# Performance work log

Hardware: AMD Instinct MI355X
Metric: run time of the kernel (lower is better)

## Reference

```python
import jax, jax.numpy as jnp
import numpy as np

# --- static config (matches init_kwargs) ---
B, S, DIM = 1, 2048, 1024
H, G, DK, DV = 16, 4, 64, 64
HPG = H // G
L, D, LSEL, NSEL, W = 32, 16, 64, 16, 512
NCMP = (S - L) // D + 1            # number of compressed blocks over full prefill
J = S // LSEL                      # number of selection blocks
GH = 32                            # gate hidden
NEG = -1e30


def rope(x, pos):
    # x: [B, S, N, Dh]; llama-style half rotation
    Dh = x.shape[-1]
    inv = 1.0 / (10000.0 ** (np.arange(0, Dh, 2) / Dh))
    ang = pos[:, None] * inv[None, :]                      # [S, Dh/2]
    cos = jnp.asarray(np.cos(ang), jnp.float32)[None, :, None, :]
    sin = jnp.asarray(np.sin(ang), jnp.float32)[None, :, None, :]
    x1, x2 = jnp.split(x, 2, axis=-1)
    return jnp.concatenate([x1 * cos - x2 * sin, x2 * cos + x1 * sin], axis=-1)


def masked_softmax(s, m):
    p = jax.nn.softmax(jnp.where(m, s, NEG), axis=-1)
    # rows with no visible keys produce 0 output (empty attention)
    return jnp.where(jnp.any(m, axis=-1, keepdims=True), p, 0.0)


def setup_inputs() -> dict:
    key = jax.random.key(0)
    ks = jax.random.split(key, 12)
    def w(k, shape, fan):
        return jax.random.normal(k, shape, jnp.float32) / np.sqrt(fan)
    return {
        'x': jax.random.normal(ks[0], (B, S, DIM), jnp.float32),
        'W_Q': w(ks[1], (DIM, H * DK), DIM),
        'W_K_sel': w(ks[2], (DIM, G * DK), DIM),
        'W_V_sel': w(ks[3], (DIM, G * DV), DIM),
        'W_K_win': w(ks[4], (DIM, G * DK), DIM),
        'W_V_win': w(ks[5], (DIM, G * DV), DIM),
        'W_K_cmp': w(ks[6], (DIM, G * DK), DIM),
        'W_V_cmp': w(ks[7], (DIM, G * DV), DIM),
        'W_out': w(ks[8], (H * DV, DIM), H * DV),
        'gate_w1': w(ks[9], (DK, GH), DK),
        'gate_b1': jnp.zeros((GH,), jnp.float32),
        'gate_w2': 0.1 * jax.random.normal(ks[10], (GH, 3), jnp.float32),
        'gate_b2': jnp.zeros((3,), jnp.float32),
    }


def reference(x, W_Q, W_K_sel, W_V_sel, W_K_win, W_V_win, W_K_cmp, W_V_cmp,
              W_out, gate_w1, gate_b1, gate_w2, gate_b2):
    pos = np.arange(S)
    s_ = np.arange(S)
    scale = 1.0 / np.sqrt(DK)

    Q = rope((x @ W_Q).reshape(B, S, H, DK), pos).reshape(B, S, G, HPG, DK)

    def proj_kv(Wk, Wv):
        K = rope((x @ Wk).reshape(B, S, G, DK), pos).transpose(0, 2, 1, 3)  # [B,G,S,Dk]
        V = (x @ Wv).reshape(B, S, G, DV).transpose(0, 2, 1, 3)            # [B,G,S,Dv]
        return K, V

    K_sel, V_sel = proj_kv(W_K_sel, W_V_sel)
    K_win, V_win = proj_kv(W_K_win, W_V_win)
    K_cr, V_cr = proj_kv(W_K_cmp, W_V_cmp)

    # --- compressed branch: avg-pool (len L, stride D) of roped K / raw V ---
    bidx = np.arange(NCMP)[:, None] * D + np.arange(L)[None, :]   # [NCMP, L]
    K_cmp = K_cr[:, :, bidx].mean(axis=3)                         # [B,G,NCMP,Dk]
    V_cmp = V_cr[:, :, bidx].mean(axis=3)
    vis_c = (np.arange(NCMP)[None, :] * D + L) <= (s_[:, None] + 1)  # block fully in past
    sc_c = jnp.einsum('bsghd,bgcd->bsghc', Q, K_cmp) * scale
    p_cmp = masked_softmax(sc_c, jnp.asarray(vis_c)[None, :, None, None, :])
    O_cmp = jnp.einsum('bsghc,bgce->bsghe', p_cmp, V_cmp)

    # --- map compressed probs -> selection-block scores (overlap fractions) ---
    i0 = np.arange(NCMP)[:, None] * D
    j0 = np.arange(J)[None, :] * LSEL
    ov = np.maximum(0, np.minimum(i0 + L, j0 + LSEL) - np.maximum(i0, j0)) / L
    p_grp = jnp.einsum('bsghc,cj->bsgj', p_cmp, jnp.asarray(ov, np.float32))  # sum over heads in group

    vis_j = (np.arange(J)[None, :] * LSEL) <= s_[:, None]
    forced = (np.arange(J)[None, :] == 0) | (np.arange(J)[None, :] == (s_ // LSEL)[:, None])
    score = jnp.where(jnp.asarray(vis_j)[None, :, None, :], p_grp, NEG)
    score = jnp.where(jnp.asarray(forced)[None, :, None, :], 1e9, score)  # force block 0 + current block
    topj = jax.lax.top_k(score, NSEL)[1]                                   # [B,S,G,NSEL]
    blk = jax.nn.one_hot(topj, J, dtype=jnp.float32).sum(axis=-2) > 0      # [B,S,G,J]

    tok2blk = np.repeat(np.arange(J), LSEL)[:S]
    causal = s_[:, None] >= s_[None, :]                                    # u <= t
    sel_mask = blk[:, :, :, tok2blk] & jnp.asarray(causal)[None, :, None, :]  # [B,S,G,S]
    sc_s = jnp.einsum('bsghd,bgud->bsghu', Q, K_sel) * scale
    O_sel = jnp.einsum('bsghu,bgue->bsghe',
                       masked_softmax(sc_s, sel_mask[:, :, :, None, :]), V_sel)

    # --- sliding window branch ---
    win_mask = causal & (s_[None, :] > s_[:, None] - W)
    sc_w = jnp.einsum('bsghd,bgud->bsghu', Q, K_win) * scale
    O_win = jnp.einsum('bsghu,bgue->bsghe',
                       masked_softmax(sc_w, jnp.asarray(win_mask)[None, :, None, None, :]), V_win)

    # --- gating MLP on head-pooled query per group ---
    gl = jax.nn.silu(Q.mean(axis=3) @ gate_w1 + gate_b1) @ gate_w2 + gate_b2  # [B,S,G,3]
    pg = jax.nn.softmax(gl, axis=-1)
    t2 = jax.lax.top_k(gl, 2)[0]
    peaked = (t2[..., 0] - t2[..., 1]) > 50.0
    gates = jnp.where(peaked[..., None],
                      jax.nn.one_hot(jnp.argmax(gl, axis=-1), 3, dtype=gl.dtype), pg)

    O = (gates[..., 0, None, None] * O_cmp
         + gates[..., 1, None, None] * O_sel
         + gates[..., 2, None, None] * O_win)          # [B,S,G,h,Dv]
    return O.reshape(B, S, H * DV) @ W_out
```

## Files before the change

### kernel.cpp

```cpp
#include <hip/hip_runtime.h>
#include <math.h>

#define S 2048
#define DIM 1024
#define H 16
#define G 4
#define HPG 4
#define DK 64
#define DV 64
#define NCMP 127
#define JBLK 32
#define NSEL 16
#define WWIN 512
#define GH 32
#define SCL2 0.18033688011112042f

typedef __attribute__((ext_vector_type(8))) __bf16 bf16x8;
typedef __attribute__((ext_vector_type(4))) float f32x4;

__device__ __forceinline__ unsigned short f2bf(float f) {
  unsigned u = __float_as_uint(f);
  unsigned r = (u + 0x7FFFu + ((u >> 16) & 1u)) >> 16;
  return (unsigned short)r;
}

__device__ __forceinline__ unsigned short f2bf_hw(float f) {
  __bf16 b = (__bf16)f;
  return *(unsigned short*)&b;
}

__device__ __forceinline__ float bf2f(unsigned short u) {
  return __uint_as_float((unsigned)u << 16);
}

__device__ __forceinline__ f32x4 mfma16(bf16x8 a, bf16x8 b, f32x4 c) {
  return __builtin_amdgcn_mfma_f32_16x16x32_bf16(a, b, c, 0, 0, 0);
}

__global__ void rope_table(float* __restrict__ cosT, float* __restrict__ sinT) {
  int idx = blockIdx.x * blockDim.x + threadIdx.x;
  if (idx >= S * 32) return;
  int s = idx >> 5, i = idx & 31;
  double inv = pow(10000.0, -2.0 * (double)i / 64.0);
  double ang = (double)s * inv;
  cosT[idx] = (float)cos(ang);
  sinT[idx] = (float)sin(ang);
}

__device__ __forceinline__ void gemm_body_k(const float* __restrict__ A,
                                            const float* __restrict__ B,
                                            float* __restrict__ C,
                                            int N, int K, int bm, int bn,
                                            int kS, int kE,
                                            float* As, float* Bs) {
  int tid = threadIdx.x;
  int tr = tid >> 4, tc = tid & 15;
  float acc[4][4] = {{0.f}};
  int arow = tid >> 2;
  int kba = (tid & 3) << 3;
  int brow = tid >> 4;
  int bcol = (tid & 15) << 2;
  const float* Ab = A + (size_t)(bm * 64) * K;
  const float* Bb = B + bn * 64;

  float4 a0 = *(const float4*)(Ab + (size_t)arow * K + kS + kba);
  float4 a1 = *(const float4*)(Ab + (size_t)arow * K + kS + kba + 4);
  float4 b0 = *(const float4*)(Bb + (size_t)(kS + brow) * N + bcol);
  float4 b1 = *(const float4*)(Bb + (size_t)(kS + brow + 16) * N + bcol);

  for (int k0 = kS; k0 < kE; k0 += 32) {
    __syncthreads();
    {
      float av[8] = {a0.x, a0.y, a0.z, a0.w, a1.x, a1.y, a1.z, a1.w};
#pragma unroll
      for (int i = 0; i < 8; ++i) {
        int k = kba + i;
        As[k * 64 + (arow ^ (((k >> 3) & 3) << 3))] = av[i];
      }
      *(float4*)&Bs[brow * 64 + bcol] = b0;
      *(float4*)&Bs[(brow + 16) * 64 + bcol] = b1;
    }
    __syncthreads();
    if (k0 + 32 < kE) {
      a0 = *(const float4*)(Ab + (size_t)arow * K + k0 + 32 + kba);
      a1 = *(const float4*)(Ab + (size_t)arow * K + k0 + 32 + kba + 4);
      b0 = *(const float4*)(Bb + (size_t)(k0 + 32 + brow) * N + bcol);
      b1 = *(const float4*)(Bb + (size_t)(k0 + 32 + brow + 16) * N + bcol);
    }
#pragma unroll
    for (int kk = 0; kk < 32; ++kk) {
      float4 a = *(const float4*)&As[kk * 64 + ((tr << 2) ^ (((kk >> 3) & 3) << 3))];
      float4 b = *(const float4*)&Bs[kk * 64 + (tc << 2)];
      acc[0][0] += a.x * b.x; acc[0][1] += a.x * b.y; acc[0][2] += a.x * b.z; acc[0][3] += a.x * b.w;
      acc[1][0] += a.y * b.x; acc[1][1] += a.y * b.y; acc[1][2] += a.y * b.z; acc[1][3] += a.y * b.w;
      acc[2][0] += a.z * b.x; acc[2][1] += a.z * b.y; acc[2][2] += a.z * b.z; acc[2][3] += a.z * b.w;
      acc[3][0] += a.w * b.x; acc[3][1] += a.w * b.y; acc[3][2] += a.w * b.z; acc[3][3] += a.w * b.w;
    }
  }
  for (int i = 0; i < 4; ++i)
    for (int jj = 0; jj < 4; ++jj)
      C[(size_t)(bm * 64 + (tr << 2) + i) * N + bn * 64 + (tc << 2) + jj] = acc[i][jj];
}

__global__ __launch_bounds__(256) void gemm_qk(const float* __restrict__ x,
                                               const float* __restrict__ W_Q,
                                               const float* __restrict__ W_Kc,
                                               float* __restrict__ Pq,
                                               float* __restrict__ Pk) {
  __shared__ float As[32 * 64];
  __shared__ float Bs[32 * 64];
  int ct = blockIdx.x, bm = blockIdx.y, z = blockIdx.z;
  int kS = z * 512, kE = kS + 512;
  if (ct < 16)
    gemm_body_k(x, W_Q, Pq + (size_t)z * S * 1024, 1024, DIM, bm, ct, kS, kE, As, Bs);
  else
    gemm_body_k(x, W_Kc, Pk + (size_t)z * S * 256, 256, DIM, bm, ct - 16, kS, kE, As, Bs);
}

__global__ __launch_bounds__(256) void reduce_rope(
    const float* __restrict__ Pq, const float* __restrict__ Pk,
    const float* __restrict__ cosT, const float* __restrict__ sinT,
    float* __restrict__ Qb, unsigned short* __restrict__ Qbf,
    float* __restrict__ Kcr) {
  int idx = blockIdx.x * 256 + threadIdx.x;
  const int NQ = S * H * 32;
  if (idx < NQ) {
    int i = idx & 31;
    int rest = idx >> 5;
    int h = rest & 15;
    int s = rest >> 4;
    size_t base = (size_t)s * 1024 + h * 64 + i;
    float a1 = Pq[base] + Pq[(size_t)S * 1024 + base];
    float a2 = Pq[base + 32] + Pq[(size_t)S * 1024 + base + 32];
    float c = cosT[s * 32 + i], sn = sinT[s * 32 + i];
    float q1 = a1 * c - a2 * sn, q2 = a2 * c + a1 * sn;
    Qb[base] = q1;
    Qb[base + 32] = q2;
    Qbf[base] = f2bf(q1);
    Qbf[base + 32] = f2bf(q2);
  } else {
    int j = idx - NQ;
    if (j >= S * G * 32) return;
    int i = j & 31;
    int rest = j >> 5;
    int g = rest & 3;
    int s = rest >> 2;
    size_t base = (size_t)s * 256 + g * 64 + i;
    float a1 = Pk[base] + Pk[(size_t)S * 256 + base];
    float a2 = Pk[base + 32] + Pk[(size_t)S * 256 + base + 32];
    float c = cosT[s * 32 + i], sn = sinT[s * 32 + i];
    Kcr[base] = a1 * c - a2 * sn;
    Kcr[base + 32] = a2 * c + a1 * sn;
  }
}

__global__ __launch_bounds__(256) void fconv(const float* __restrict__ a,
                                             unsigned short* __restrict__ b) {
  int idx = (blockIdx.x * 256 + threadIdx.x) * 8;
  float4 x = *(const float4*)&a[idx];
  float4 y = *(const float4*)&a[idx + 4];
  union { unsigned short us[8]; float4 f4; } t;
  t.us[0] = f2bf(x.x); t.us[1] = f2bf(x.y); t.us[2] = f2bf(x.z); t.us[3] = f2bf(x.w);
  t.us[4] = f2bf(y.x); t.us[5] = f2bf(y.y); t.us[6] = f2bf(y.z); t.us[7] = f2bf(y.w);
  *(float4*)&b[idx] = t.f4;
}

__global__ __launch_bounds__(256) void wtrans(const float* __restrict__ W0,
                                              const float* __restrict__ W1,
                                              const float* __restrict__ W2,
                                              const float* __restrict__ W3,
                                              const float* __restrict__ W4,
                                              unsigned short* __restrict__ Wt) {
  __shared__ float t[64][65];
  int k0 = blockIdx.x * 64;
  int n0 = blockIdx.y * 64;
  int m = blockIdx.z;
  const float* W = (m == 0) ? W0 : (m == 1) ? W1 : (m == 2) ? W2 : (m == 3) ? W3 : W4;
  int tid = threadIdx.x;
  int rr = tid >> 4, c4 = (tid & 15) * 4;
#pragma unroll
  for (int e = 0; e < 4; ++e) {
    int row = rr + e * 16;
    float4 v = *(const float4*)(W + (size_t)(k0 + row) * 256 + n0 + c4);
    t[c4 + 0][row] = v.x;
    t[c4 + 1][row] = v.y;
    t[c4 + 2][row] = v.z;
    t[c4 + 3][row] = v.w;
  }
  __syncthreads();
#pragma unroll
  for (int e = 0; e < 2; ++e) {
    int flat = tid + e * 256;
    int col = flat >> 3, kc = (flat & 7) * 8;
    union { unsigned short us[8]; float4 f4; } u;
#pragma unroll
    for (int i = 0; i < 8; ++i) u.us[i] = f2bf(t[col][kc + i]);
    *(float4*)(Wt + ((size_t)m * 256 + n0 + col) * 1024 + k0 + kc) = u.f4;
  }
}

__global__ __launch_bounds__(256) void wtrans_o(const float* __restrict__ W,
                                                unsigned short* __restrict__ Wt) {
  __shared__ float t[64][65];
  int k0 = blockIdx.x * 64;
  int n0 = blockIdx.y * 64;
  int tid = threadIdx.x;
  int rr = tid >> 4, c4 = (tid & 15) * 4;
#pragma unroll
  for (int e = 0; e < 4; ++e) {
    int row = rr + e * 16;
    float4 v = *(const float4*)(W + (size_t)(k0 + row) * 1024 + n0 + c4);
    t[c4 + 0][row] = v.x;
    t[c4 + 1][row] = v.y;
    t[c4 + 2][row] = v.z;
    t[c4 + 3][row] = v.w;
  }
  __syncthreads();
#pragma unroll
  for (int e = 0; e < 2; ++e) {
    int flat = tid + e * 256;
    int col = flat >> 3, kc = (flat & 7) * 8;
    union { unsigned short us[8]; float4 f4; } u;
#pragma unroll
    for (int i = 0; i < 8; ++i) u.us[i] = f2bf(t[col][kc + i]);
    *(float4*)(Wt + (size_t)(n0 + col) * 1024 + k0 + kc) = u.f4;
  }
}

__global__ __launch_bounds__(256) void proj_bf16(
    const unsigned short* __restrict__ xb, const unsigned short* __restrict__ Wt,
    const float* __restrict__ cosT, const float* __restrict__ sinT,
    unsigned short* __restrict__ Kb_s, unsigned short* __restrict__ Vt_s,
    unsigned short* __restrict__ Kb_w, unsigned short* __restrict__ Vt_w,
    unsigned short* __restrict__ Vt_c) {
  __shared__ unsigned short xs[64 * 64];
  __shared__ unsigned short ws[64 * 64];
  int s0 = blockIdx.x * 64;
  int g = blockIdx.y;
  int mat = blockIdx.z;
  int tid = threadIdx.x, w = tid >> 6, lane = tid & 63;
  int l15 = lane & 15, lg = lane >> 4;
  int rswz = (l15 & 7) << 3;
  bool isV = (mat == 1) || (mat == 3) || (mat == 4);
  const unsigned short* wt = Wt + ((size_t)mat * 256 + g * 64) * 1024;

  f32x4 acc[4];
#pragma unroll
  for (int nt = 0; nt < 4; ++nt) acc[nt] = (f32x4){0.f, 0.f, 0.f, 0.f};

  for (int k0 = 0; k0 < DIM; k0 += 64) {
#pragma unroll
    for (int e = 0; e < 2; ++e) {
      int flat = tid + e * 256;
      int row = flat >> 3, cc = flat & 7;
      int dsti = row * 64 + ((cc ^ (row & 7)) << 3);
      *(float4*)&xs[dsti] = *(const float4*)(xb + (size_t)(s0 + row) * DIM + k0 + cc * 8);
      *(float4*)&ws[dsti] = *(const float4*)(wt + (size_t)row * DIM + k0 + cc * 8);
    }
    __syncthreads();
    const unsigned short* aP = isV ? ws : xs;
    const unsigned short* bP = isV ? xs : ws;
    int arow = w * 16 + l15;
    bf16x8 af[2];
#pragma unroll
    for (int kc = 0; kc < 2; ++kc)
      af[kc] = *(const bf16x8*)&aP[(arow * 64 + kc * 32 + lg * 8) ^ rswz];
#pragma unroll
    for (int nt = 0; nt < 4; ++nt) {
      int brow = nt * 16 + l15;
      bf16x8 b0 = *(const bf16x8*)&bP[(brow * 64 + lg * 8) ^ rswz];
      bf16x8 b1 = *(const bf16x8*)&bP[(brow * 64 + 32 + lg * 8) ^ rswz];
      acc[nt] = mfma16(af[0], b0, acc[nt]);
      acc[nt] = mfma16(af[1], b1, acc[nt]);
    }
    __syncthreads();
  }

  if (!isV) {
    unsigned short* Kb = (mat == 0) ? Kb_s : Kb_w;
#pragma unroll
    for (int rr = 0; rr < 4; ++rr) {
      int tok = s0 + w * 16 + lg * 4 + rr;
#pragma unroll
      for (int p = 0; p < 2; ++p) {
        int i = p * 16 + l15;
        float c = cosT[tok * 32 + i], sn = sinT[tok * 32 + i];
        float x1 = acc[p][rr], x2 = acc[p + 2][rr];
        Kb[((size_t)g * S + tok) * 64 + i] = f2bf(x1 * c - x2 * sn);
        Kb[((size_t)g * S + tok) * 64 + i + 32] = f2bf(x2 * c + x1 * sn);
      }
    }
  } else {
    unsigned short* Vt = (mat == 1) ? Vt_s : (mat == 3) ? Vt_w : Vt_c;
#pragma unroll
    for (int rr = 0; rr < 4; ++rr) {
      int col = w * 16 + lg * 4 + rr;
#pragma unroll
      for (int nt = 0; nt < 4; ++nt) {
        int tok = s0 + nt * 16 + l15;
        Vt[((size_t)g * 64 + col) * S + tok] = f2bf(acc[nt][rr]);
      }
    }
  }
}

__global__ __launch_bounds__(256) void gemm_out(const unsigned short* __restrict__ Ob,
                                                const unsigned short* __restrict__ Wt,
                                                float* __restrict__ out) {
  __shared__ unsigned short xs[64 * 64];
  __shared__ unsigned short ws[64 * 64];
  int s0 = blockIdx.x * 64;
  int n0 = blockIdx.y * 64;
  int tid = threadIdx.x, w = tid >> 6, lane = tid & 63;
  int l15 = lane & 15, lg = lane >> 4;
  int rswz = (l15 & 7) << 3;

  f32x4 acc[4];
#pragma unroll
  for (int nt = 0; nt < 4; ++nt) acc[nt] = (f32x4){0.f, 0.f, 0.f, 0.f};

  for (int k0 = 0; k0 < DIM; k0 += 64) {
#pragma unroll
    for (int e = 0; e < 2; ++e) {
      int flat = tid + e * 256;
      int row = flat >> 3, cc = flat & 7;
      int dsti = row * 64 + ((cc ^ (row & 7)) << 3);
      *(float4*)&xs[dsti] = *(const float4*)(Ob + (size_t)(s0 + row) * DIM + k0 + cc * 8);
      *(float4*)&ws[dsti] = *(const float4*)(Wt + (size_t)(n0 + row) * DIM + k0 + cc * 8);
    }
    __syncthreads();
    int arow = w * 16 + l15;
    bf16x8 af0 = *(const bf16x8*)&xs[(arow * 64 + lg * 8) ^ rswz];
    bf16x8 af1 = *(const bf16x8*)&xs[(arow * 64 + 32 + lg * 8) ^ rswz];
#pragma unroll
    for (int nt = 0; nt < 4; ++nt) {
      int brow = nt * 16 + l15;
      bf16x8 b0 = *(const bf16x8*)&ws[(brow * 64 + lg * 8) ^ rswz];
      bf16x8 b1 = *(const bf16x8*)&ws[(brow * 64 + 32 + lg * 8) ^ rswz];
      acc[nt] = mfma16(af0, b0, acc[nt]);
      acc[nt] = mfma16(af1, b1, acc[nt]);
    }
    __syncthreads();
  }

#pragma unroll
  for (int nt = 0; nt < 4; ++nt)
#pragma unroll
    for (int rr = 0; rr < 4; ++rr)
      out[(size_t)(s0 + w * 16 + lg * 4 + rr) * 1024 + n0 + nt * 16 + l15] =
          acc[nt][rr];
}

__global__ void pool_cmp(const float* __restrict__ Kcr,
                         const unsigned short* __restrict__ Vtc,
                         float* __restrict__ Kc, float* __restrict__ Vc) {
  int c = blockIdx.x, g = blockIdx.y, d = threadIdx.x;
  float sk = 0.f, sv = 0.f;
  const unsigned short* vrow = Vtc + ((size_t)g * 64 + d) * S + c * 16;
  for (int l = 0; l < 32; ++l) {
    sk += Kcr[(size_t)((c * 16 + l) * G + g) * 64 + d];
    sv += bf2f(vrow[l]);
  }
  Kc[(size_t)(g * NCMP + c) * 64 + d] = sk * (1.f / 32.f);
  Vc[(size_t)(g * NCMP + c) * 64 + d] = sv * (1.f / 32.f);
}

__global__ __launch_bounds__(256) void cmp_attn(const float* __restrict__ Q,
                                                const float* __restrict__ Kc,
                                                const float* __restrict__ Vc,
                                                float* __restrict__ Ocmp,
                                                unsigned int* __restrict__ selm) {
  int s = blockIdx.x, g = blockIdx.y;
  __shared__ float q4[4][64];
  __shared__ float sc[4][128];
  __shared__ float pg[JBLK];
  int tid = threadIdx.x;
  int nvis = (s >= 31) ? (((s - 31) >> 4) + 1) : 0;
  {
    int h = tid >> 6, d = tid & 63;
    q4[h][d] = Q[(size_t)(s * H + g * HPG + h) * 64 + d];
  }
  __syncthreads();

  if (tid < 128) {
    int c = tid;
    if (c < nvis) {
      float a0 = 0.f, a1 = 0.f, a2 = 0.f, a3 = 0.f;
      const float* kr = &Kc[(size_t)(g * NCMP + c) * 64];
#pragma unroll 4
      for (int kk = 0; kk < 16; ++kk) {
        float4 kv = *(const float4*)&kr[kk * 4];
        float4 q0 = *(const float4*)&q4[0][kk * 4];
        float4 q1 = *(const float4*)&q4[1][kk * 4];
        float4 q2 = *(const float4*)&q4[2][kk * 4];
        float4 q3 = *(const float4*)&q4[3][kk * 4];
        a0 += q0.x * kv.x + q0.y * kv.y + q0.z * kv.z + q0.w * kv.w;
        a1 += q1.x * kv.x + q1.y * kv.y + q1.z * kv.z + q1.w * kv.w;
        a2 += q2.x * kv.x + q2.y * kv.y + q2.z * kv.z + q2.w * kv.w;
        a3 += q3.x * kv.x + q3.y * kv.y + q3.z * kv.z + q3.w * kv.w;
      }
      sc[0][c] = a0 * 0.125f;
      sc[1][c] = a1 * 0.125f;
      sc[2][c] = a2 * 0.125f;
      sc[3][c] = a3 * 0.125f;
    } else {
      sc[0][c] = -INFINITY;
      sc[1][c] = -INFINITY;
      sc[2][c] = -INFINITY;
      sc[3][c] = -INFINITY;
    }
  }
  __syncthreads();

  int w = tid >> 6, lane = tid & 63;
  {
    float v0 = sc[w][lane];
    float v1 = (lane + 64 < NCMP) ? sc[w][lane + 64] : -INFINITY;
    float m = fmaxf(v0, v1);
    for (int off = 32; off; off >>= 1) m = fmaxf(m, __shfl_xor(m, off));
    float e0 = (m > -INFINITY && v0 > -INFINITY) ? expf(v0 - m) : 0.f;
    float e1 = (m > -INFINITY && v1 > -INFINITY) ? expf(v1 - m) : 0.f;
    float sum = e0 + e1;
    for (int off = 32; off; off >>= 1) sum += __shfl_xor(sum, off);
    float inv = (sum > 0.f) ? 1.f / sum : 0.f;
    sc[w][lane] = e0 * inv;
    if (lane + 64 < NCMP) sc[w][lane + 64] = e1 * inv;
    if (lane == 63) sc[w][127] = 0.f;
  }
  __syncthreads();

  {
    int h = tid >> 6, d = tid & 63;
    float o = 0.f;
#pragma unroll 4
    for (int c = 0; c < nvis; ++c) o += sc[h][c] * Vc[(size_t)(g * NCMP + c) * 64 + d];
    Ocmp[(size_t)(s * H + g * HPG + h) * 64 + d] = o;
  }

  if (tid < JBLK) {
    int j = tid;
    float a = 0.f;
#pragma unroll
    for (int h = 0; h < 4; ++h) {
      const float* row = sc[h];
      float v = row[4 * j] + row[4 * j + 1] + row[4 * j + 2] + 0.5f * row[4 * j + 3];
      if (j > 0) v += 0.5f * row[4 * j - 1];
      a += v;
    }
    pg[j] = a;
  }
  __syncthreads();

  if (tid < 64) {
    int j = tid & 31;
    int cur = s >> 6;
    float v = (j * 64 <= s) ? pg[j] : -1e30f;
    if (j == 0 || j == cur) v = 1e9f;
    unsigned int mask = 0;
#pragma unroll 1
    for (int n = 0; n < NSEL; ++n) {
      float bv = v;
      int bj = j;
#pragma unroll
      for (int off = 1; off < 32; off <<= 1) {
        float ov = __shfl_xor(bv, off);
        int oj = __shfl_xor(bj, off);
        if (ov > bv || (ov == bv && oj < bj)) { bv = ov; bj = oj; }
      }
      mask |= 1u << bj;
      if (j == bj) v = -INFINITY;
    }
    if (tid == 0) selm[(size_t)s * G + g] = mask;
  }
}

__global__ __launch_bounds__(256) void attn_fused(
    const unsigned short* __restrict__ Qbf,
    const unsigned short* __restrict__ Kbs, const unsigned short* __restrict__ Vts,
    const unsigned short* __restrict__ Kbw, const unsigned short* __restrict__ Vtw,
    const unsigned int* __restrict__ selm,
    float* __restrict__ Osel, float* __restrict__ Owin) {
  __shared__ unsigned short Kl[64 * 64];
  __shared__ unsigned short Vt[64 * 64];
  __shared__ unsigned short Pl[4][16 * 64];
  __shared__ unsigned int sel_l[16];
  __shared__ int blist[JBLK];
  __shared__ int nB_s;

  int t0 = blockIdx.x * 16;
  int g = blockIdx.y;
  int mode = blockIdx.z;
  int tid = threadIdx.x;
  int w = tid >> 6, lane = tid & 63;
  int l15 = lane & 15, lg = lane >> 4;
  int rswz = (l15 & 7) << 3;
  int jdiag = t0 >> 6;

  const unsigned short* Kb = mode ? Kbw : Kbs;
  const unsigned short* Vtb = mode ? Vtw : Vts;
  float* O = mode ? Owin : Osel;

  if (mode == 0 && tid < 16) sel_l[tid] = selm[(t0 + tid) * G + g];
  __syncthreads();
  if (tid == 0) {
    int n = 0;
    if (mode == 0) {
      unsigned int un = 0;
      for (int i = 0; i < 16; ++i) un |= sel_l[i];
      for (int j = 0; j <= jdiag; ++j)
        if ((un >> j) & 1u) blist[n++] = j;
    } else {
      int lo = t0 - (WWIN - 1);
      int j0 = (lo > 0) ? (lo >> 6) : 0;
      for (int j = j0; j <= jdiag; ++j) blist[n++] = j;
    }
    nB_s = n;
  }
  __syncthreads();
  int nB = nB_s;

  int tok = t0 + l15;
  bf16x8 qf[2];
  {
    const unsigned short* qb = Qbf + ((size_t)tok * H + g * HPG + w) * 64;
    qf[0] = *(const bf16x8*)(qb + lg * 8);
    qf[1] = *(const bf16x8*)(qb + 32 + lg * 8);
  }

  float mrun = -INFINITY, lrun = 0.f;
  f32x4 oacc[4];
#pragma unroll
  for (int dt = 0; dt < 4; ++dt) oacc[dt] = (f32x4){0.f, 0.f, 0.f, 0.f};

  for (int b = 0; b < nB; ++b) {
    int j = blist[b];
    int ku = j * 64;

    {
      const unsigned short* src = Kb + ((size_t)g * S + ku) * 64;
#pragma unroll
      for (int c2 = 0; c2 < 2; ++c2) {
        int chunk = tid + c2 * 256;
        int key = chunk >> 3, cc = chunk & 7;
        *(float4*)&Kl[key * 64 + ((cc ^ (key & 7)) << 3)] =
            *(const float4*)(src + chunk * 8);
      }
#pragma unroll
      for (int c2 = 0; c2 < 2; ++c2) {
        int chunk = tid + c2 * 256;
        int dim = chunk >> 3, cc = chunk & 7;
        *(float4*)&Vt[dim * 64 + ((cc ^ (dim & 7)) << 3)] =
            *(const float4*)(Vtb + ((size_t)g * 64 + dim) * S + ku + cc * 8);
      }
    }
    __syncthreads();

    f32x4 sf[4];
#pragma unroll
    for (int kt = 0; kt < 4; ++kt) sf[kt] = (f32x4){0.f, 0.f, 0.f, 0.f};
#pragma unroll
    for (int kt = 0; kt < 4; ++kt) {
      int krow = kt * 16 + l15;
      bf16x8 kf0 = *(const bf16x8*)&Kl[(krow * 64 + lg * 8) ^ rswz];
      bf16x8 kf1 = *(const bf16x8*)&Kl[(krow * 64 + 32 + lg * 8) ^ rswz];
      sf[kt] = mfma16(kf0, qf[0], sf[kt]);
      sf[kt] = mfma16(kf1, qf[1], sf[kt]);
    }

    bool bsel = true;
    if (mode == 0) bsel = ((sel_l[l15] >> j) & 1u) != 0;
    float sv2[4][4];
    if (j == jdiag) {
#pragma unroll
      for (int kt = 0; kt < 4; ++kt)
#pragma unroll
        for (int rr = 0; rr < 4; ++rr) {
          int u = ku + kt * 16 + lg * 4 + rr;
          sv2[kt][rr] = (u <= tok) ? sf[kt][rr] * SCL2 : -INFINITY;
        }
    } else if (mode == 1 && (ku + WWIN <= t0 + 15)) {
#pragma unroll
      for (int kt = 0; kt < 4; ++kt)
#pragma unroll
        for (int rr = 0; rr < 4; ++rr) {
          int u = ku + kt * 16 + lg * 4 + rr;
          sv2[kt][rr] = (u + WWIN > tok) ? sf[kt][rr] * SCL2 : -INFINITY;
        }
    } else {
#pragma unroll
      for (int kt = 0; kt < 4; ++kt)
#pragma unroll
        for (int rr = 0; rr < 4; ++rr) sv2[kt][rr] = sf[kt][rr] * SCL2;
    }

    float pmax = -INFINITY;
#pragma unroll
    for (int kt = 0; kt < 4; ++kt)
#pragma unroll
      for (int rr = 0; rr < 4; ++rr) pmax = fmaxf(pmax, sv2[kt][rr]);
    pmax = fmaxf(pmax, __shfl_xor(pmax, 16));
    pmax = fmaxf(pmax, __shfl_xor(pmax, 32));
    if (mode == 0 && !bsel) pmax = -INFINITY;

    if (__any(pmax > mrun)) {
      float mnew = fmaxf(mrun, pmax);
      float mc = (mnew == -INFINITY) ? 0.f : mnew;
      float fac = exp2f(mrun - mc);
      mrun = mnew;
      lrun *= fac;
#pragma unroll
      for (int dt = 0; dt < 4; ++dt)
#pragma unroll
        for (int rr = 0; rr < 4; ++rr) oacc[dt][rr] *= fac;
    }
    float mcb = (mode == 0 && !bsel) ? INFINITY
                                     : ((mrun == -INFINITY) ? 0.f : mrun);

    float psum = 0.f;
    unsigned short pb[16];
#pragma unroll
    for (int kt = 0; kt < 4; ++kt)
#pragma unroll
      for (int rr = 0; rr < 4; ++rr) {
        float e = exp2f(sv2[kt][rr] - mcb);
        psum += e;
        pb[kt * 4 + rr] = f2bf_hw(e);
      }
    psum += __shfl_xor(psum, 16);
    psum += __shfl_xor(psum, 32);
    lrun += psum;

    {
      unsigned short* pw = &Pl[w][0];
#pragma unroll
      for (int kt = 0; kt < 4; ++kt) {
        int idx = (l15 * 64 + kt * 16 + lg * 4) ^ rswz;
        unsigned int lo = (unsigned)pb[kt * 4] | ((unsigned)pb[kt * 4 + 1] << 16);
        unsigned int hi = (unsigned)pb[kt * 4 + 2] | ((unsigned)pb[kt * 4 + 3] << 16);
        *(uint2*)&pw[idx] = make_uint2(lo, hi);
      }
    }

#pragma unroll
    for (int kc = 0; kc < 2; ++kc) {
      bf16x8 pf = *(const bf16x8*)&Pl[w][(l15 * 64 + kc * 32 + lg * 8) ^ rswz];
#pragma unroll
      for (int dt = 0; dt < 4; ++dt) {
        bf16x8 vf = *(const bf16x8*)&Vt[((dt * 16 + l15) * 64 + kc * 32 + lg * 8) ^ rswz];
        oacc[dt] = mfma16(vf, pf, oacc[dt]);
      }
    }
    __syncthreads();
  }

  {
    float inv = (lrun > 0.f) ? 1.f / lrun : 0.f;
    float* ob = O + ((size_t)tok * H + g * HPG + w) * 64;
#pragma unroll
    for (int dt = 0; dt < 4; ++dt) {
      float4 v;
      v.x = oacc[dt][0] * inv;
      v.y = oacc[dt][1] * inv;
      v.z = oacc[dt][2] * inv;
      v.w = oacc[dt][3] * inv;
      *(float4*)(ob + dt * 16 + lg * 4) = v;
    }
  }
}

__global__ void gate_kernel(const float* __restrict__ Q, const float* __restrict__ w1,
                            const float* __restrict__ b1, const float* __restrict__ w2,
                            const float* __restrict__ b2, float* __restrict__ gates) {
  int idx = blockIdx.x * blockDim.x + threadIdx.x;
  if (idx >= S * G) return;
  int s = idx >> 2, g = idx & 3;
  float qm[64];
#pragma unroll
  for (int d = 0; d < 64; ++d) {
    float a = 0.f;
    for (int hp = 0; hp < HPG; ++hp) a += Q[(size_t)(s * H + g * HPG + hp) * 64 + d];
    qm[d] = a * 0.25f;
  }
  float gl[3] = {b2[0], b2[1], b2[2]};
  for (int j = 0; j < GH; ++j) {
    float z = b1[j];
    for (int d = 0; d < 64; ++d) z += qm[d] * w1[d * GH + j];
    float sl = z / (1.f + expf(-z));
    gl[0] += sl * w2[j * 3 + 0];
    gl[1] += sl * w2[j * 3 + 1];
    gl[2] += sl * w2[j * 3 + 2];
  }
  float m = fmaxf(gl[0], fmaxf(gl[1], gl[2]));
  float e0 = expf(gl[0] - m), e1 = expf(gl[1] - m), e2 = expf(gl[2] - m);
  float inv = 1.f / (e0 + e1 + e2);
  float p0 = e0 * inv, p1 = e1 * inv, p2 = e2 * inv;
  int am = (gl[0] >= gl[1] && gl[0] >= gl[2]) ? 0 : ((gl[1] >= gl[2]) ? 1 : 2);
  float t1 = (am == 0) ? fmaxf(gl[1], gl[2]) : ((am == 1) ? fmaxf(gl[0], gl[2]) : fmaxf(gl[0], gl[1]));
  if (m - t1 > 50.f) {
    p0 = (am == 0) ? 1.f : 0.f;
    p1 = (am == 1) ? 1.f : 0.f;
    p2 = (am == 2) ? 1.f : 0.f;
  }
  gates[idx * 3 + 0] = p0;
  gates[idx * 3 + 1] = p1;
  gates[idx * 3 + 2] = p2;
}

__global__ void combine(const float* __restrict__ Oc, const float* __restrict__ Os,
                        const float* __restrict__ Ow, const float* __restrict__ gates,
                        unsigned short* __restrict__ Ob) {
  int idx = blockIdx.x * blockDim.x + threadIdx.x;
  if (idx >= S * H * DV) return;
  int h = (idx >> 6) & 15;
  int s = idx >> 10;
  int g = h >> 2;
  const float* gp = &gates[(size_t)(s * G + g) * 3];
  Ob[idx] = f2bf(gp[0] * Oc[idx] + gp[1] * Os[idx] + gp[2] * Ow[idx]);
}

extern "C" void kernel_launch(void* const* d_in, const int* in_sizes, int n_in,
                              void* d_out, int out_size, void* d_ws, size_t ws_size,
                              hipStream_t stream) {
  const float* x = (const float*)d_in[0];
  const float* W_Q = (const float*)d_in[1];
  const float* W_K_sel = (const float*)d_in[2];
  const float* W_V_sel = (const float*)d_in[3];
  const float* W_K_win = (const float*)d_in[4];
  const float* W_V_win = (const float*)d_in[5];
  const float* W_K_cmp = (const float*)d_in[6];
  const float* W_V_cmp = (const float*)d_in[7];
  const float* W_out = (const float*)d_in[8];
  const float* gw1 = (const float*)d_in[9];
  const float* gb1 = (const float*)d_in[10];
  const float* gw2 = (const float*)d_in[11];
  const float* gb2 = (const float*)d_in[12];

  float* w = (float*)d_ws;
  float* cosT = w;  w += S * 32;
  float* sinT = w;  w += S * 32;
  float* Qb   = w;  w += S * H * DK;
  float* Kcr  = w;  w += S * G * DK;
  float* Kc   = w;  w += G * NCMP * DK;
  float* Vc   = w;  w += G * NCMP * DV;
  float* Ocmp = w;  w += S * H * DV;
  float* Osel = w;  w += S * H * DV;
  float* Owin = w;  w += S * H * DV;
  float* gates= w;  w += S * G * 3;
  unsigned int* selm = (unsigned int*)w;  w += S * G;
  unsigned short* Kbf_s = (unsigned short*)w;  w += (size_t)G * S * 64 / 2;
  unsigned short* Kbf_w = (unsigned short*)w;  w += (size_t)G * S * 64 / 2;
  unsigned short* Vt_s  = (unsigned short*)w;  w += (size_t)G * S * 64 / 2;
  unsigned short* Vt_w  = (unsigned short*)w;  w += (size_t)G * S * 64 / 2;
  unsigned short* Vt_c  = (unsigned short*)w;  w += (size_t)G * S * 64 / 2;
  unsigned short* Qbf   = (unsigned short*)w;  w += (size_t)S * H * 64 / 2;
  unsigned short* xb    = (unsigned short*)w;  w += (size_t)S * DIM / 2;
  unsigned short* Wt    = (unsigned short*)w;  w += (size_t)5 * 256 * DIM / 2;
  unsigned short* Ob    = (unsigned short*)w;  w += (size_t)S * H * DV / 2;
  unsigned short* WtO   = (unsigned short*)w;  w += (size_t)DIM * DIM / 2;

  float* Pq = Ocmp;
  float* Pk = Owin;

  rope_table<<<(S * 32 + 255) / 256, 256, 0, stream>>>(cosT, sinT);
  fconv<<<(S * DIM) / 2048, 256, 0, stream>>>(x, xb);
  wtrans<<<dim3(DIM / 64, 4, 5), 256, 0, stream>>>(W_K_sel, W_V_sel, W_K_win,
                                                   W_V_win, W_V_cmp, Wt);
  wtrans_o<<<dim3(DIM / 64, DIM / 64), 256, 0, stream>>>(W_out, WtO);

  gemm_qk<<<dim3(20, S / 64, 2), 256, 0, stream>>>(x, W_Q, W_K_cmp, Pq, Pk);
  reduce_rope<<<(S * (H + G) * 32) / 256, 256, 0, stream>>>(Pq, Pk, cosT, sinT,
                                                            Qb, Qbf, Kcr);

  proj_bf16<<<dim3(S / 64, G, 5), 256, 0, stream>>>(xb, Wt, cosT, sinT, Kbf_s, Vt_s,
                                                    Kbf_w, Vt_w, Vt_c);

  pool_cmp<<<dim3(NCMP, G), 64, 0, stream>>>(Kcr, Vt_c, Kc, Vc);

  cmp_attn<<<dim3(S, G), 256, 0, stream>>>(Qb, Kc, Vc, Ocmp, selm);
  attn_fused<<<dim3(S / 16, G, 2), 256, 0, stream>>>(Qbf, Kbf_s, Vt_s, Kbf_w, Vt_w,
                                                     selm, Osel, Owin);

  gate_kernel<<<(S * G + 255) / 256, 256, 0, stream>>>(Qb, gw1, gb1, gw2, gb2, gates);
  combine<<<(S * H * DV + 255) / 256, 256, 0, stream>>>(Ocmp, Osel, Owin, gates, Ob);

  gemm_out<<<dim3(S / 64, DIM / 64), 256, 0, stream>>>(Ob, WtO, (float*)d_out);
}
```

Baseline: 307.1 us.

## Fuse independent kernels into heterogeneous launches to overlap QK/proj and cmp/window attention

```diff
diff --git a/kernel.cpp b/kernel.cpp
--- a/kernel.cpp
+++ b/kernel.cpp
@@ -52,7 +52,7 @@
                                             float* __restrict__ C,
                                             int N, int K, int bm, int bn,
                                             int kS, int kE,
-                                            float* As, float* Bs) {
+                                            float* As , float* Bs ) {
   int tid = threadIdx.x;
   int tr = tid >> 4, tc = tid & 15;
   float acc[4][4] = {{0.f}};
@@ -102,19 +102,113 @@
       C[(size_t)(bm * 64 + (tr << 2) + i) * N + bn * 64 + (tc << 2) + jj] = acc[i][jj];
 }
 
-__global__ __launch_bounds__(256) void gemm_qk(const float* __restrict__ x,
-                                               const float* __restrict__ W_Q,
-                                               const float* __restrict__ W_Kc,
-                                               float* __restrict__ Pq,
-                                               float* __restrict__ Pk) {
-  __shared__ float As[32 * 64];
-  __shared__ float Bs[32 * 64];
-  int ct = blockIdx.x, bm = blockIdx.y, z = blockIdx.z;
-  int kS = z * 512, kE = kS + 512;
-  if (ct < 16)
-    gemm_body_k(x, W_Q, Pq + (size_t)z * S * 1024, 1024, DIM, bm, ct, kS, kE, As, Bs);
-  else
-    gemm_body_k(x, W_Kc, Pk + (size_t)z * S * 256, 256, DIM, bm, ct - 16, kS, kE, As, Bs);
+__device__ __forceinline__ void proj_body(
+    const unsigned short* __restrict__ xb, const unsigned short* __restrict__ Wt,
+    const float* __restrict__ cosT, const float* __restrict__ sinT,
+    unsigned short* __restrict__ Kb_s, unsigned short* __restrict__ Vt_s,
+    unsigned short* __restrict__ Kb_w, unsigned short* __restrict__ Vt_w,
+    unsigned short* __restrict__ Vt_c,
+    int s0, int g, int mat, unsigned short* xs, unsigned short* ws) {
+  int tid = threadIdx.x, w = tid >> 6, lane = tid & 63;
+  int l15 = lane & 15, lg = lane >> 4;
+  int rswz = (l15 & 7) << 3;
+  bool isV = (mat == 1) || (mat == 3) || (mat == 4);
+  const unsigned short* wt = Wt + ((size_t)mat * 256 + g * 64) * 1024;
+
+  f32x4 acc[4];
+#pragma unroll
+  for (int nt = 0; nt < 4; ++nt) acc[nt] = (f32x4){0.f, 0.f, 0.f, 0.f};
+
+  for (int k0 = 0; k0 < DIM; k0 += 64) {
+#pragma unroll
+    for (int e = 0; e < 2; ++e) {
+      int flat = tid + e * 256;
+      int row = flat >> 3, cc = flat & 7;
+      int dsti = row * 64 + ((cc ^ (row & 7)) << 3);
+      *(float4*)&xs[dsti] = *(const float4*)(xb + (size_t)(s0 + row) * DIM + k0 + cc * 8);
+      *(float4*)&ws[dsti] = *(const float4*)(wt + (size_t)row * DIM + k0 + cc * 8);
+    }
+    __syncthreads();
+    const unsigned short* aP = isV ? ws : xs;
+    const unsigned short* bP = isV ? xs : ws;
+    int arow = w * 16 + l15;
+    bf16x8 af[2];
+#pragma unroll
+    for (int kc = 0; kc < 2; ++kc)
+      af[kc] = *(const bf16x8*)&aP[(arow * 64 + kc * 32 + lg * 8) ^ rswz];
+#pragma unroll
+    for (int nt = 0; nt < 4; ++nt) {
+      int brow = nt * 16 + l15;
+      bf16x8 b0 = *(const bf16x8*)&bP[(brow * 64 + lg * 8) ^ rswz];
+      bf16x8 b1 = *(const bf16x8*)&bP[(brow * 64 + 32 + lg * 8) ^ rswz];
+      acc[nt] = mfma16(af[0], b0, acc[nt]);
+      acc[nt] = mfma16(af[1], b1, acc[nt]);
+    }
+    __syncthreads();
+  }
+
+  if (!isV) {
+    unsigned short* Kb = (mat == 0) ? Kb_s : Kb_w;
+#pragma unroll
+    for (int rr = 0; rr < 4; ++rr) {
+      int tok = s0 + w * 16 + lg * 4 + rr;
+#pragma unroll
+      for (int p = 0; p < 2; ++p) {
+        int i = p * 16 + l15;
+        float c = cosT[tok * 32 + i], sn = sinT[tok * 32 + i];
+        float x1 = acc[p][rr], x2 = acc[p + 2][rr];
+        Kb[((size_t)g * S + tok) * 64 + i] = f2bf(x1 * c - x2 * sn);
+        Kb[((size_t)g * S + tok) * 64 + i + 32] = f2bf(x2 * c + x1 * sn);
+      }
+    }
+  } else {
+    unsigned short* Vt = (mat == 1) ? Vt_s : (mat == 3) ? Vt_w : Vt_c;
+#pragma unroll
+    for (int rr = 0; rr < 4; ++rr) {
+      int col = w * 16 + lg * 4 + rr;
+#pragma unroll
+      for (int nt = 0; nt < 4; ++nt) {
+        int tok = s0 + nt * 16 + l15;
+        Vt[((size_t)g * 64 + col) * S + tok] = f2bf(acc[nt][rr]);
+      }
+    }
+  }
+}
+
+__global__ __launch_bounds__(256) void qk_proj(
+    const float* __restrict__ x, const float* __restrict__ W_Q,
+    const float* __restrict__ W_Kc, float* __restrict__ Pq, float* __restrict__ Pk,
+    const unsigned short* __restrict__ xb, const unsigned short* __restrict__ Wt,
+    const float* __restrict__ cosT, const float* __restrict__ sinT,
+    unsigned short* __restrict__ Kb_s, unsigned short* __restrict__ Vt_s,
+    unsigned short* __restrict__ Kb_w, unsigned short* __restrict__ Vt_w,
+    unsigned short* __restrict__ Vt_c) {
+  __shared__ __align__(16) float lds_f[4096];
+  int bid = blockIdx.x;
+  int r = bid % 3;
+  if (r < 2) {
+    int gid = (bid / 3) * 2 + r;
+    int z = gid / 640;
+    int rem = gid % 640;
+    int ct = rem % 20;
+    int bm = rem / 20;
+    int kS = z * 512, kE = kS + 512;
+    float* As = lds_f;
+    float* Bs = lds_f + 2048;
+    if (ct < 16)
+      gemm_body_k(x, W_Q, Pq + (size_t)z * S * 1024, 1024, DIM, bm, ct, kS, kE, As, Bs);
+    else
+      gemm_body_k(x, W_Kc, Pk + (size_t)z * S * 256, 256, DIM, bm, ct - 16, kS, kE, As, Bs);
+  } else {
+    int pid = bid / 3;
+    int s0b = pid % 32;
+    int g = (pid / 32) % 4;
+    int mat = pid / 128;
+    unsigned short* xs = (unsigned short*)lds_f;
+    unsigned short* ws = xs + 4096;
+    proj_body(xb, Wt, cosT, sinT, Kb_s, Vt_s, Kb_w, Vt_w, Vt_c, s0b * 64, g, mat,
+              xs, ws);
+  }
 }
 
 __global__ __launch_bounds__(256) void reduce_rope(
@@ -227,83 +321,6 @@
   }
 }
 
-__global__ __launch_bounds__(256) void proj_bf16(
-    const unsigned short* __restrict__ xb, const unsigned short* __restrict__ Wt,
-    const float* __restrict__ cosT, const float* __restrict__ sinT,
-    unsigned short* __restrict__ Kb_s, unsigned short* __restrict__ Vt_s,
-    unsigned short* __restrict__ Kb_w, unsigned short* __restrict__ Vt_w,
-    unsigned short* __restrict__ Vt_c) {
-  __shared__ unsigned short xs[64 * 64];
-  __shared__ unsigned short ws[64 * 64];
-  int s0 = blockIdx.x * 64;
-  int g = blockIdx.y;
-  int mat = blockIdx.z;
-  int tid = threadIdx.x, w = tid >> 6, lane = tid & 63;
-  int l15 = lane & 15, lg = lane >> 4;
-  int rswz = (l15 & 7) << 3;
-  bool isV = (mat == 1) || (mat == 3) || (mat == 4);
-  const unsigned short* wt = Wt + ((size_t)mat * 256 + g * 64) * 1024;
-
-  f32x4 acc[4];
-#pragma unroll
-  for (int nt = 0; nt < 4; ++nt) acc[nt] = (f32x4){0.f, 0.f, 0.f, 0.f};
-
-  for (int k0 = 0; k0 < DIM; k0 += 64) {
-#pragma unroll
-    for (int e = 0; e < 2; ++e) {
-      int flat = tid + e * 256;
-      int row = flat >> 3, cc = flat & 7;
-      int dsti = row * 64 + ((cc ^ (row & 7)) << 3);
-      *(float4*)&xs[dsti] = *(const float4*)(xb + (size_t)(s0 + row) * DIM + k0 + cc * 8);
-      *(float4*)&ws[dsti] = *(const float4*)(wt + (size_t)row * DIM + k0 + cc * 8);
-    }
-    __syncthreads();
-    const unsigned short* aP = isV ? ws : xs;
-    const unsigned short* bP = isV ? xs : ws;
-    int arow = w * 16 + l15;
-    bf16x8 af[2];
-#pragma unroll
-    for (int kc = 0; kc < 2; ++kc)
-      af[kc] = *(const bf16x8*)&aP[(arow * 64 + kc * 32 + lg * 8) ^ rswz];
-#pragma unroll
-    for (int nt = 0; nt < 4; ++nt) {
-      int brow = nt * 16 + l15;
-      bf16x8 b0 = *(const bf16x8*)&bP[(brow * 64 + lg * 8) ^ rswz];
-      bf16x8 b1 = *(const bf16x8*)&bP[(brow * 64 + 32 + lg * 8) ^ rswz];
-      acc[nt] = mfma16(af[0], b0, acc[nt]);
-      acc[nt] = mfma16(af[1], b1, acc[nt]);
-    }
-    __syncthreads();
-  }
-
-  if (!isV) {
-    unsigned short* Kb = (mat == 0) ? Kb_s : Kb_w;
-#pragma unroll
-    for (int rr = 0; rr < 4; ++rr) {
-      int tok = s0 + w * 16 + lg * 4 + rr;
-#pragma unroll
-      for (int p = 0; p < 2; ++p) {
-        int i = p * 16 + l15;
-        float c = cosT[tok * 32 + i], sn = sinT[tok * 32 + i];
-        float x1 = acc[p][rr], x2 = acc[p + 2][rr];
-        Kb[((size_t)g * S + tok) * 64 + i] = f2bf(x1 * c - x2 * sn);
-        Kb[((size_t)g * S + tok) * 64 + i + 32] = f2bf(x2 * c + x1 * sn);
-      }
-    }
-  } else {
-    unsigned short* Vt = (mat == 1) ? Vt_s : (mat == 3) ? Vt_w : Vt_c;
-#pragma unroll
-    for (int rr = 0; rr < 4; ++rr) {
-      int col = w * 16 + lg * 4 + rr;
-#pragma unroll
-      for (int nt = 0; nt < 4; ++nt) {
-        int tok = s0 + nt * 16 + l15;
-        Vt[((size_t)g * 64 + col) * S + tok] = f2bf(acc[nt][rr]);
-      }
-    }
-  }
-}
-
 __global__ __launch_bounds__(256) void gemm_out(const unsigned short* __restrict__ Ob,
                                                 const unsigned short* __restrict__ Wt,
                                                 float* __restrict__ out) {
@@ -365,20 +382,19 @@
   Vc[(size_t)(g * NCMP + c) * 64 + d] = sv * (1.f / 32.f);
 }
 
-__global__ __launch_bounds__(256) void cmp_attn(const float* __restrict__ Q,
-                                                const float* __restrict__ Kc,
-                                                const float* __restrict__ Vc,
-                                                float* __restrict__ Ocmp,
-                                                unsigned int* __restrict__ selm) {
-  int s = blockIdx.x, g = blockIdx.y;
-  __shared__ float q4[4][64];
-  __shared__ float sc[4][128];
-  __shared__ float pg[JBLK];
+__device__ __forceinline__ void cmp_body(const float* __restrict__ Q,
+                                         const float* __restrict__ Kc,
+                                         const float* __restrict__ Vc,
+                                         float* __restrict__ Ocmp,
+                                         unsigned int* __restrict__ selm,
+                                         int s, int g,
+                                         float* q4 , float* sc ,
+                                         float* pg ) {
   int tid = threadIdx.x;
   int nvis = (s >= 31) ? (((s - 31) >> 4) + 1) : 0;
   {
     int h = tid >> 6, d = tid & 63;
-    q4[h][d] = Q[(size_t)(s * H + g * HPG + h) * 64 + d];
+    q4[h * 64 + d] = Q[(size_t)(s * H + g * HPG + h) * 64 + d];
   }
   __syncthreads();
 
@@ -390,32 +406,32 @@
 #pragma unroll 4
       for (int kk = 0; kk < 16; ++kk) {
         float4 kv = *(const float4*)&kr[kk * 4];
-        float4 q0 = *(const float4*)&q4[0][kk * 4];
-        float4 q1 = *(const float4*)&q4[1][kk * 4];
-        float4 q2 = *(const float4*)&q4[2][kk * 4];
-        float4 q3 = *(const float4*)&q4[3][kk * 4];
+        float4 q0 = *(const float4*)&q4[0 * 64 + kk * 4];
+        float4 q1 = *(const float4*)&q4[1 * 64 + kk * 4];
+        float4 q2 = *(const float4*)&q4[2 * 64 + kk * 4];
+        float4 q3 = *(const float4*)&q4[3 * 64 + kk * 4];
         a0 += q0.x * kv.x + q0.y * kv.y + q0.z * kv.z + q0.w * kv.w;
         a1 += q1.x * kv.x + q1.y * kv.y + q1.z * kv.z + q1.w * kv.w;
         a2 += q2.x * kv.x + q2.y * kv.y + q2.z * kv.z + q2.w * kv.w;
         a3 += q3.x * kv.x + q3.y * kv.y + q3.z * kv.z + q3.w * kv.w;
       }
-      sc[0][c] = a0 * 0.125f;
-      sc[1][c] = a1 * 0.125f;
-      sc[2][c] = a2 * 0.125f;
-      sc[3][c] = a3 * 0.125f;
+      sc[0 * 128 + c] = a0 * 0.125f;
+      sc[1 * 128 + c] = a1 * 0.125f;
+      sc[2 * 128 + c] = a2 * 0.125f;
+      sc[3 * 128 + c] = a3 * 0.125f;
     } else {
-      sc[0][c] = -INFINITY;
-      sc[1][c] = -INFINITY;
-      sc[2][c] = -INFINITY;
-      sc[3][c] = -INFINITY;
+      sc[0 * 128 + c] = -INFINITY;
+      sc[1 * 128 + c] = -INFINITY;
+      sc[2 * 128 + c] = -INFINITY;
+      sc[3 * 128 + c] = -INFINITY;
     }
   }
   __syncthreads();
 
   int w = tid >> 6, lane = tid & 63;
   {
-    float v0 = sc[w][lane];
-    float v1 = (lane + 64 < NCMP) ? sc[w][lane + 64] : -INFINITY;
+    float v0 = sc[w * 128 + lane];
+    float v1 = (lane + 64 < NCMP) ? sc[w * 128 + lane + 64] : -INFINITY;
     float m = fmaxf(v0, v1);
     for (int off = 32; off; off >>= 1) m = fmaxf(m, __shfl_xor(m, off));
     float e0 = (m > -INFINITY && v0 > -INFINITY) ? expf(v0 - m) : 0.f;
@@ -423,9 +439,9 @@
     float sum = e0 + e1;
     for (int off = 32; off; off >>= 1) sum += __shfl_xor(sum, off);
     float inv = (sum > 0.f) ? 1.f / sum : 0.f;
-    sc[w][lane] = e0 * inv;
-    if (lane + 64 < NCMP) sc[w][lane + 64] = e1 * inv;
-    if (lane == 63) sc[w][127] = 0.f;
+    sc[w * 128 + lane] = e0 * inv;
+    if (lane + 64 < NCMP) sc[w * 128 + lane + 64] = e1 * inv;
+    if (lane == 63) sc[w * 128 + 127] = 0.f;
   }
   __syncthreads();
 
@@ -433,7 +449,8 @@
     int h = tid >> 6, d = tid & 63;
     float o = 0.f;
 #pragma unroll 4
-    for (int c = 0; c < nvis; ++c) o += sc[h][c] * Vc[(size_t)(g * NCMP + c) * 64 + d];
+    for (int c = 0; c < nvis; ++c)
+      o += sc[h * 128 + c] * Vc[(size_t)(g * NCMP + c) * 64 + d];
     Ocmp[(size_t)(s * H + g * HPG + h) * 64 + d] = o;
   }
 
@@ -442,7 +459,7 @@
     float a = 0.f;
 #pragma unroll
     for (int h = 0; h < 4; ++h) {
-      const float* row = sc[h];
+      const float* row = &sc[h * 128];
       float v = row[4 * j] + row[4 * j + 1] + row[4 * j + 2] + 0.5f * row[4 * j + 3];
       if (j > 0) v += 0.5f * row[4 * j - 1];
       a += v;
@@ -474,37 +491,24 @@
   }
 }
 
-__global__ __launch_bounds__(256) void attn_fused(
-    const unsigned short* __restrict__ Qbf,
-    const unsigned short* __restrict__ Kbs, const unsigned short* __restrict__ Vts,
-    const unsigned short* __restrict__ Kbw, const unsigned short* __restrict__ Vtw,
-    const unsigned int* __restrict__ selm,
-    float* __restrict__ Osel, float* __restrict__ Owin) {
-  __shared__ unsigned short Kl[64 * 64];
-  __shared__ unsigned short Vt[64 * 64];
-  __shared__ unsigned short Pl[4][16 * 64];
-  __shared__ unsigned int sel_l[16];
-  __shared__ int blist[JBLK];
-  __shared__ int nB_s;
-
-  int t0 = blockIdx.x * 16;
-  int g = blockIdx.y;
-  int mode = blockIdx.z;
+template <int MODE>
+__device__ __forceinline__ void attn_body(
+    const unsigned short* __restrict__ Qbf, const unsigned short* __restrict__ Kb,
+    const unsigned short* __restrict__ Vtb, const unsigned int* __restrict__ selm,
+    float* __restrict__ O, int t0, int g,
+    unsigned short* Kl, unsigned short* Vt, unsigned short* Pl,
+    unsigned int* sel_l, int* blist, int* nB_p) {
   int tid = threadIdx.x;
   int w = tid >> 6, lane = tid & 63;
   int l15 = lane & 15, lg = lane >> 4;
   int rswz = (l15 & 7) << 3;
   int jdiag = t0 >> 6;
 
-  const unsigned short* Kb = mode ? Kbw : Kbs;
-  const unsigned short* Vtb = mode ? Vtw : Vts;
-  float* O = mode ? Owin : Osel;
-
-  if (mode == 0 && tid < 16) sel_l[tid] = selm[(t0 + tid) * G + g];
+  if (MODE == 0 && tid < 16) sel_l[tid] = selm[(t0 + tid) * G + g];
   __syncthreads();
   if (tid == 0) {
     int n = 0;
-    if (mode == 0) {
+    if (MODE == 0) {
       unsigned int un = 0;
       for (int i = 0; i < 16; ++i) un |= sel_l[i];
       for (int j = 0; j <= jdiag; ++j)
@@ -514,10 +518,10 @@
       int j0 = (lo > 0) ? (lo >> 6) : 0;
       for (int j = j0; j <= jdiag; ++j) blist[n++] = j;
     }
-    nB_s = n;
+    *nB_p = n;
   }
   __syncthreads();
-  int nB = nB_s;
+  int nB = *nB_p;
 
   int tok = t0 + l15;
   bf16x8 qf[2];
@@ -568,7 +572,7 @@
     }
 
     bool bsel = true;
-    if (mode == 0) bsel = ((sel_l[l15] >> j) & 1u) != 0;
+    if (MODE == 0) bsel = ((sel_l[l15] >> j) & 1u) != 0;
     float sv2[4][4];
     if (j == jdiag) {
 #pragma unroll
@@ -578,7 +582,7 @@
           int u = ku + kt * 16 + lg * 4 + rr;
           sv2[kt][rr] = (u <= tok) ? sf[kt][rr] * SCL2 : -INFINITY;
         }
-    } else if (mode == 1 && (ku + WWIN <= t0 + 15)) {
+    } else if (MODE == 1 && (ku + WWIN <= t0 + 15)) {
 #pragma unroll
       for (int kt = 0; kt < 4; ++kt)
 #pragma unroll
@@ -600,7 +604,7 @@
       for (int rr = 0; rr < 4; ++rr) pmax = fmaxf(pmax, sv2[kt][rr]);
     pmax = fmaxf(pmax, __shfl_xor(pmax, 16));
     pmax = fmaxf(pmax, __shfl_xor(pmax, 32));
-    if (mode == 0 && !bsel) pmax = -INFINITY;
+    if (MODE == 0 && !bsel) pmax = -INFINITY;
 
     if (__any(pmax > mrun)) {
       float mnew = fmaxf(mrun, pmax);
@@ -613,7 +617,7 @@
 #pragma unroll
         for (int rr = 0; rr < 4; ++rr) oacc[dt][rr] *= fac;
     }
-    float mcb = (mode == 0 && !bsel) ? INFINITY
+    float mcb = (MODE == 0 && !bsel) ? INFINITY
                                      : ((mrun == -INFINITY) ? 0.f : mrun);
 
     float psum = 0.f;
@@ -631,7 +635,7 @@
     lrun += psum;
 
     {
-      unsigned short* pw = &Pl[w][0];
+      unsigned short* pw = Pl + w * 1024;
 #pragma unroll
       for (int kt = 0; kt < 4; ++kt) {
         int idx = (l15 * 64 + kt * 16 + lg * 4) ^ rswz;
@@ -643,7 +647,7 @@
 
 #pragma unroll
     for (int kc = 0; kc < 2; ++kc) {
-      bf16x8 pf = *(const bf16x8*)&Pl[w][(l15 * 64 + kc * 32 + lg * 8) ^ rswz];
+      bf16x8 pf = *(const bf16x8*)&Pl[w * 1024 + ((l15 * 64 + kc * 32 + lg * 8) ^ rswz)];
 #pragma unroll
       for (int dt = 0; dt < 4; ++dt) {
         bf16x8 vf = *(const bf16x8*)&Vt[((dt * 16 + l15) * 64 + kc * 32 + lg * 8) ^ rswz];
@@ -666,6 +670,50 @@
       *(float4*)(ob + dt * 16 + lg * 4) = v;
     }
   }
+}
+
+__global__ __launch_bounds__(256) void cmp_win(
+    const float* __restrict__ Qb, const float* __restrict__ Kc,
+    const float* __restrict__ Vc, float* __restrict__ Ocmp,
+    unsigned int* __restrict__ selm, const unsigned short* __restrict__ Qbf,
+    const unsigned short* __restrict__ Kbw, const unsigned short* __restrict__ Vtw,
+    float* __restrict__ Owin) {
+  __shared__ __align__(16) unsigned char ldsb[24832];
+  int bid = blockIdx.x;
+  if (bid % 17 != 16) {
+    int cid = (bid / 17) * 16 + (bid % 17);
+    int s = cid >> 2, g = cid & 3;
+    float* q4 = (float*)ldsb;
+    float* sc = q4 + 256;
+    float* pg = sc + 512;
+    cmp_body(Qb, Kc, Vc, Ocmp, selm, s, g, q4, sc, pg);
+  } else {
+    int pid = bid / 17;
+    int t0 = (pid & 127) * 16;
+    int g = pid >> 7;
+    unsigned short* Kl = (unsigned short*)ldsb;
+    unsigned short* Vt = Kl + 4096;
+    unsigned short* Pl = Vt + 4096;
+    int* blist = (int*)(Pl + 4096);
+    int* nB_p = blist + JBLK;
+    attn_body<1>(Qbf, Kbw, Vtw, nullptr, Owin, t0, g, Kl, Vt, Pl, nullptr, blist,
+                 nB_p);
+  }
+}
+
+__global__ __launch_bounds__(256) void attn_sel(
+    const unsigned short* __restrict__ Qbf, const unsigned short* __restrict__ Kbs,
+    const unsigned short* __restrict__ Vts, const unsigned int* __restrict__ selm,
+    float* __restrict__ Osel) {
+  __shared__ unsigned short Kl[4096];
+  __shared__ unsigned short Vt[4096];
+  __shared__ unsigned short Pl[4096];
+  __shared__ unsigned int sel_l[16];
+  __shared__ int blist[JBLK];
+  __shared__ int nB_s;
+  int t0 = blockIdx.x * 16;
+  int g = blockIdx.y;
+  attn_body<0>(Qbf, Kbs, Vts, selm, Osel, t0, g, Kl, Vt, Pl, sel_l, blist, &nB_s);
 }
 
 __global__ void gate_kernel(const float* __restrict__ Q, const float* __restrict__ w1,
@@ -767,18 +815,15 @@
                                                    W_V_win, W_V_cmp, Wt);
   wtrans_o<<<dim3(DIM / 64, DIM / 64), 256, 0, stream>>>(W_out, WtO);
 
-  gemm_qk<<<dim3(20, S / 64, 2), 256, 0, stream>>>(x, W_Q, W_K_cmp, Pq, Pk);
+  qk_proj<<<1920, 256, 0, stream>>>(x, W_Q, W_K_cmp, Pq, Pk, xb, Wt, cosT, sinT,
+                                    Kbf_s, Vt_s, Kbf_w, Vt_w, Vt_c);
   reduce_rope<<<(S * (H + G) * 32) / 256, 256, 0, stream>>>(Pq, Pk, cosT, sinT,
                                                             Qb, Qbf, Kcr);
 
-  proj_bf16<<<dim3(S / 64, G, 5), 256, 0, stream>>>(xb, Wt, cosT, sinT, Kbf_s, Vt_s,
-                                                    Kbf_w, Vt_w, Vt_c);
-
   pool_cmp<<<dim3(NCMP, G), 64, 0, stream>>>(Kcr, Vt_c, Kc, Vc);
 
-  cmp_attn<<<dim3(S, G), 256, 0, stream>>>(Qb, Kc, Vc, Ocmp, selm);
-  attn_fused<<<dim3(S / 16, G, 2), 256, 0, stream>>>(Qbf, Kbf_s, Vt_s, Kbf_w, Vt_w,
-                                                     selm, Osel, Owin);
+  cmp_win<<<8704, 256, 0, stream>>>(Qb, Kc, Vc, Ocmp, selm, Qbf, Kbf_w, Vt_w, Owin);
+  attn_sel<<<dim3(S / 16, G), 256, 0, stream>>>(Qbf, Kbf_s, Vt_s, selm, Osel);
 
   gate_kernel<<<(S * G + 255) / 256, 256, 0, stream>>>(Qb, gw1, gb1, gw2, gb2, gates);
   combine<<<(S * H * DV + 255) / 256, 256, 0, stream>>>(Ocmp, Osel, Owin, gates, Ob);
```

Measured after the change: 328.6 us. 7.0% more time.
